# Kernel optimization log

Hardware: AMD Instinct MI355X
Metric: run time of the kernel (lower is better)

Reference implementation:

```python
import jax, jax.numpy as jnp
import numpy as np

B, S, H, NH = 2, 2048, 2048, 16
HD = H // NH
SCALE = 1.0 / np.sqrt(HD).astype(np.float32)


def setup_inputs() -> dict:
    key = jax.random.key(0)
    ks = jax.random.split(key, 11)
    std = 1.0 / np.sqrt(H)
    inp = {
        'query': jax.random.normal(ks[0], (B, S, H), dtype=jnp.float32),
        'key': jax.random.normal(ks[1], (B, S, H), dtype=jnp.float32),
        'value': jax.random.normal(ks[2], (B, S, H), dtype=jnp.float32),
        'Wq': jax.random.normal(ks[3], (H, H), dtype=jnp.float32) * std,
        'bq': jax.random.normal(ks[4], (H,), dtype=jnp.float32) * std,
        'Wk': jax.random.normal(ks[5], (H, H), dtype=jnp.float32) * std,
        'bk': jax.random.normal(ks[6], (H,), dtype=jnp.float32) * std,
        'Wv': jax.random.normal(ks[7], (H, H), dtype=jnp.float32) * std,
        'bv': jax.random.normal(ks[8], (H,), dtype=jnp.float32) * std,
        'Wo': jax.random.normal(ks[9], (H, H), dtype=jnp.float32) * std,
        'bo': jax.random.normal(ks[10], (H,), dtype=jnp.float32) * std,
    }
    return inp


def reference(query, key, value, Wq, bq, Wk, bk, Wv, bv, Wo, bo):
    # Linear projections (torch Linear: x @ W.T + b)
    q = query @ Wq.T + bq
    k = key @ Wk.T + bk
    v = value @ Wv.T + bv
    # [B, NH, S, HD]
    q = q.reshape(B, S, NH, HD).transpose(0, 2, 1, 3)
    k = k.reshape(B, S, NH, HD).transpose(0, 2, 1, 3)
    v = v.reshape(B, S, NH, HD).transpose(0, 2, 1, 3)
    scores = jnp.einsum('bhqd,bhkd->bhqk', q, k) * SCALE
    attn = jax.nn.softmax(scores, axis=-1)  # dropout p=0 (eval)
    ctx = jnp.einsum('bhqk,bhkd->bhqd', attn, v)
    ctx = ctx.transpose(0, 2, 1, 3).reshape(B, S, H)
    out = ctx @ Wo.T + bo
    return out
```

## Files before the change

kernel.cpp:

```cpp
#include <hip/hip_runtime.h>


typedef __bf16 bf16_t;
typedef __bf16 bf16x8 __attribute__((ext_vector_type(8)));
typedef float  f32x4  __attribute__((ext_vector_type(4)));

#define DEVI __device__ __forceinline__

DEVI void async_copy16(const void* gsrc, void* ldst) {
  __builtin_amdgcn_global_load_lds(
      (const __attribute__((address_space(1))) unsigned int*)gsrc,
      (__attribute__((address_space(3))) unsigned int*)ldst, 16, 0, 0);
}

constexpr int Bc = 2, Sc = 2048, Hc = 2048, NHc = 16, HDc = 128;
constexpr float SCALE_F = 0.088388347648318447f;
constexpr int PSTR = 136;

DEVI void cast_body(const float* __restrict__ in, bf16_t* __restrict__ out) {
  int i = (blockIdx.x * 256 + threadIdx.x) * 8;
  float4 f0 = *(const float4*)(in + i);
  float4 f1 = *(const float4*)(in + i + 4);
  union { bf16_t h[8]; uint4 u; } o;
  o.h[0] = (bf16_t)f0.x; o.h[1] = (bf16_t)f0.y;
  o.h[2] = (bf16_t)f0.z; o.h[3] = (bf16_t)f0.w;
  o.h[4] = (bf16_t)f1.x; o.h[5] = (bf16_t)f1.y;
  o.h[6] = (bf16_t)f1.z; o.h[7] = (bf16_t)f1.w;
  *(uint4*)(out + i) = o.u;
}

__global__ void cast3(const float* __restrict__ a, const float* __restrict__ b,
                      const float* __restrict__ c, bf16_t* __restrict__ oa,
                      bf16_t* __restrict__ ob, bf16_t* __restrict__ oc) {
  const float* src = blockIdx.y == 0 ? a : blockIdx.y == 1 ? b : c;
  bf16_t* dst = blockIdx.y == 0 ? oa : blockIdx.y == 1 ? ob : oc;
  cast_body(src, dst);
}

__global__ void cast4(const float* __restrict__ a, const float* __restrict__ b,
                      const float* __restrict__ c, const float* __restrict__ d,
                      bf16_t* __restrict__ oa, bf16_t* __restrict__ ob,
                      bf16_t* __restrict__ oc, bf16_t* __restrict__ od) {
  const float* src = blockIdx.y == 0 ? a : blockIdx.y == 1 ? b
                   : blockIdx.y == 2 ? c : d;
  bf16_t* dst = blockIdx.y == 0 ? oa : blockIdx.y == 1 ? ob
              : blockIdx.y == 2 ? oc : od;
  cast_body(src, dst);
}

template <int M, int N, int K, int OUT_MODE>
__global__ __launch_bounds__(256, 2) void gemm_bt(const bf16_t* __restrict__ A,
                                                  const bf16_t* __restrict__ Bw,
                                                  const float* __restrict__ bias,
                                                  void* __restrict__ Cout,
                                                  float scale) {
  constexpr int BM = 128, BN = 128, BK = 64;
  __shared__ __align__(16) bf16_t As[BM * BK];
  __shared__ __align__(16) bf16_t Bs[BN * BK];
  const int tid = threadIdx.x;
  const int lane = tid & 63;
  const int wave = tid >> 6;
  const int bm = blockIdx.x & (M / BM - 1);
  const int bn = blockIdx.x / (M / BM);
  const int wm = wave >> 1, wn = wave & 1;
  const int quad = lane >> 4, l15 = lane & 15;

  int s_r[4], s_c[4];
#pragma unroll
  for (int i = 0; i < 4; ++i) {
    int seg = wave * 4 + i;
    int r = seg * 8 + (lane >> 3);
    s_r[i] = r;
    s_c[i] = (lane & 7) ^ (r & 7);
  }
  const bf16_t* Abase = A + (size_t)bm * BM * K;
  const bf16_t* Bbase = Bw + (size_t)bn * BN * K;

  f32x4 zero4 = {0.f, 0.f, 0.f, 0.f};
  f32x4 acc[4][4];
#pragma unroll
  for (int i = 0; i < 4; ++i)
#pragma unroll
    for (int j = 0; j < 4; ++j) acc[i][j] = zero4;

  int arow[4], brow[4];
#pragma unroll
  for (int t = 0; t < 4; ++t) {
    arow[t] = wm * 64 + t * 16 + l15;
    brow[t] = wn * 64 + t * 16 + l15;
  }

  for (int kt = 0; kt < K / BK; ++kt) {
    const int k0 = kt * BK;
#pragma unroll
    for (int i = 0; i < 4; ++i) {
      int seg = wave * 4 + i;
      async_copy16(Abase + (size_t)s_r[i] * K + k0 + s_c[i] * 8, As + seg * 512);
      async_copy16(Bbase + (size_t)s_r[i] * K + k0 + s_c[i] * 8, Bs + seg * 512);
    }
    __syncthreads();
#pragma unroll
    for (int ks = 0; ks < 2; ++ks) {
      bf16x8 af[4], bfv[4];
#pragma unroll
      for (int mt = 0; mt < 4; ++mt)
        af[mt] = *(const bf16x8*)(As + arow[mt] * 64 +
                                  (((ks * 4 + quad) ^ (arow[mt] & 7)) * 8));
#pragma unroll
      for (int nt = 0; nt < 4; ++nt)
        bfv[nt] = *(const bf16x8*)(Bs + brow[nt] * 64 +
                                   (((ks * 4 + quad) ^ (brow[nt] & 7)) * 8));
#pragma unroll
      for (int mt = 0; mt < 4; ++mt)
#pragma unroll
        for (int nt = 0; nt < 4; ++nt)
          acc[mt][nt] = __builtin_amdgcn_mfma_f32_16x16x32_bf16(
              af[mt], bfv[nt], acc[mt][nt], 0, 0, 0);
    }
    __syncthreads();
  }

  float bv[4];
#pragma unroll
  for (int nt = 0; nt < 4; ++nt) bv[nt] = bias[bn * BN + brow[nt]];

#pragma unroll
  for (int mt = 0; mt < 4; ++mt) {
    const int rbase = bm * BM + wm * 64 + mt * 16 + quad * 4;
#pragma unroll
    for (int nt = 0; nt < 4; ++nt) {
      const int col = bn * BN + brow[nt];
      if constexpr (OUT_MODE == 0) {
        bf16_t* C = (bf16_t*)Cout;
#pragma unroll
        for (int r = 0; r < 4; ++r)
          C[(size_t)(rbase + r) * N + col] = (bf16_t)((acc[mt][nt][r] + bv[nt]) * scale);
      } else if constexpr (OUT_MODE == 2) {
        float* C = (float*)Cout;
#pragma unroll
        for (int r = 0; r < 4; ++r)
          C[(size_t)(rbase + r) * N + col] = acc[mt][nt][r] + bv[nt];
      } else {
        bf16_t* C = (bf16_t*)Cout;
        const int bb = rbase >> 11;
        const int s0 = rbase & (Sc - 1);
        const int h = col >> 7, d = col & (HDc - 1);
        union { bf16_t h4[4]; uint2 u; } o;
#pragma unroll
        for (int r = 0; r < 4; ++r) o.h4[r] = (bf16_t)(acc[mt][nt][r] + bv[nt]);
        *(uint2*)(C + (((size_t)(bb * NHc + h) * HDc + d) * Sc + s0)) = o.u;
      }
    }
  }
}

__global__ __launch_bounds__(256, 1) void flash_attn(const bf16_t* __restrict__ Q,
                                                     const bf16_t* __restrict__ Kg,
                                                     const bf16_t* __restrict__ Vt,
                                                     bf16_t* __restrict__ ctx) {
  extern __shared__ char smem[];
  bf16_t* Ks = (bf16_t*)smem;
  bf16_t* Vs = (bf16_t*)(smem + 32768);
  bf16_t* Ps = (bf16_t*)(smem + 65536);

  const int tid = threadIdx.x, lane = tid & 63, wave = tid >> 6;
  const int quad = lane >> 4, l15 = lane & 15;
  const int bid = blockIdx.x;
  const int qt = bid & 15, h = (bid >> 4) & 15, b = bid >> 8;

  bf16_t* Pw = Ps + wave * (32 * PSTR);

  bf16x8 qf[2][4];
#pragma unroll
  for (int mt = 0; mt < 2; ++mt) {
    int grow = b * Sc + qt * 128 + wave * 32 + mt * 16 + l15;
    const bf16_t* qp = Q + (size_t)grow * Hc + h * HDc;
#pragma unroll
    for (int kc = 0; kc < 4; ++kc) qf[mt][kc] = *(const bf16x8*)(qp + kc * 32 + quad * 8);
  }

  f32x4 zero4 = {0.f, 0.f, 0.f, 0.f};
  f32x4 o[2][8];
#pragma unroll
  for (int mt = 0; mt < 2; ++mt)
#pragma unroll
    for (int dt = 0; dt < 8; ++dt) o[mt][dt] = zero4;
  float mrow[2][4], lrow[2][4];
#pragma unroll
  for (int mt = 0; mt < 2; ++mt)
#pragma unroll
    for (int r = 0; r < 4; ++r) { mrow[mt][r] = -1e30f; lrow[mt][r] = 0.f; }

  int st_r[8], st_c[8];
#pragma unroll
  for (int i = 0; i < 8; ++i) {
    int seg = wave * 8 + i;
    st_r[i] = seg * 4 + (lane >> 4);
    st_c[i] = (lane & 15) ^ (st_r[i] & 7);
  }
  const bf16_t* Kbase = Kg + (size_t)b * Sc * Hc + h * HDc;
  const bf16_t* Vbase = Vt + (size_t)(b * NHc + h) * HDc * Sc;

  for (int kb = 0; kb < 16; ++kb) {
#pragma unroll
    for (int i = 0; i < 8; ++i) {
      int seg = wave * 8 + i;
      async_copy16(Kbase + (size_t)(kb * 128 + st_r[i]) * Hc + st_c[i] * 8, Ks + seg * 512);
      async_copy16(Vbase + (size_t)st_r[i] * Sc + kb * 128 + st_c[i] * 8, Vs + seg * 512);
    }
    __syncthreads();

    f32x4 sf[2][8];
#pragma unroll
    for (int mt = 0; mt < 2; ++mt)
#pragma unroll
      for (int nt = 0; nt < 8; ++nt) sf[mt][nt] = zero4;
#pragma unroll
    for (int kc = 0; kc < 4; ++kc)
#pragma unroll
      for (int nt = 0; nt < 8; ++nt) {
        int kr = nt * 16 + l15;
        bf16x8 kf = *(const bf16x8*)(Ks + kr * 128 + (((kc * 4 + quad) ^ (kr & 7)) * 8));
        sf[0][nt] = __builtin_amdgcn_mfma_f32_16x16x32_bf16(qf[0][kc], kf, sf[0][nt], 0, 0, 0);
        sf[1][nt] = __builtin_amdgcn_mfma_f32_16x16x32_bf16(qf[1][kc], kf, sf[1][nt], 0, 0, 0);
      }

#pragma unroll
    for (int mt = 0; mt < 2; ++mt)
#pragma unroll
      for (int r = 0; r < 4; ++r) {
        float mx = sf[mt][0][r];
#pragma unroll
        for (int nt = 1; nt < 8; ++nt) mx = fmaxf(mx, sf[mt][nt][r]);
#pragma unroll
        for (int off = 1; off < 16; off <<= 1) mx = fmaxf(mx, __shfl_xor(mx, off));
        float mnew = fmaxf(mrow[mt][r], mx);
        float alpha = __expf(mrow[mt][r] - mnew);
        float rs = 0.f;
#pragma unroll
        for (int nt = 0; nt < 8; ++nt) {
          float p = __expf(sf[mt][nt][r] - mnew);
          sf[mt][nt][r] = p;
          rs += p;
        }
#pragma unroll
        for (int off = 1; off < 16; off <<= 1) rs += __shfl_xor(rs, off);
        lrow[mt][r] = lrow[mt][r] * alpha + rs;
        mrow[mt][r] = mnew;
#pragma unroll
        for (int dt = 0; dt < 8; ++dt) o[mt][dt][r] *= alpha;
      }

#pragma unroll
    for (int mt = 0; mt < 2; ++mt)
#pragma unroll
      for (int nt = 0; nt < 8; ++nt)
#pragma unroll
        for (int r = 0; r < 4; ++r)
          Pw[(mt * 16 + quad * 4 + r) * PSTR + nt * 16 + l15] = (bf16_t)sf[mt][nt][r];

    bf16x8 pf[2][4];
#pragma unroll
    for (int mt = 0; mt < 2; ++mt) {
      const bf16_t* pr = Pw + (mt * 16 + l15) * PSTR;
#pragma unroll
      for (int kc = 0; kc < 4; ++kc)
        pf[mt][kc] = *(const bf16x8*)(pr + kc * 32 + quad * 8);
    }

#pragma unroll
    for (int kc = 0; kc < 4; ++kc)
#pragma unroll
      for (int dt = 0; dt < 8; ++dt) {
        int vr = dt * 16 + l15;
        bf16x8 vf = *(const bf16x8*)(Vs + vr * 128 + (((kc * 4 + quad) ^ (vr & 7)) * 8));
        o[0][dt] = __builtin_amdgcn_mfma_f32_16x16x32_bf16(pf[0][kc], vf, o[0][dt], 0, 0, 0);
        o[1][dt] = __builtin_amdgcn_mfma_f32_16x16x32_bf16(pf[1][kc], vf, o[1][dt], 0, 0, 0);
      }
    __syncthreads();
  }

#pragma unroll
  for (int mt = 0; mt < 2; ++mt) {
    float rinv[4];
#pragma unroll
    for (int r = 0; r < 4; ++r) rinv[r] = 1.f / lrow[mt][r];
#pragma unroll
    for (int dt = 0; dt < 8; ++dt)
#pragma unroll
      for (int r = 0; r < 4; ++r)
        Pw[(mt * 16 + quad * 4 + r) * PSTR + dt * 16 + l15] = (bf16_t)(o[mt][dt][r] * rinv[r]);
  }
#pragma unroll
  for (int r = 0; r < 32; ++r) {
    unsigned v = *(const unsigned*)(Pw + r * PSTR + lane * 2);
    int grow = b * Sc + qt * 128 + wave * 32 + r;
    *(unsigned*)(ctx + (size_t)grow * Hc + h * HDc + lane * 2) = v;
  }
}

extern "C" void kernel_launch(void* const* d_in, const int* in_sizes, int n_in,
                              void* d_out, int out_size, void* d_ws, size_t ws_size,
                              hipStream_t stream) {
  const float* query = (const float*)d_in[0];
  const float* key_i = (const float*)d_in[1];
  const float* value = (const float*)d_in[2];
  const float* Wq = (const float*)d_in[3];
  const float* bq = (const float*)d_in[4];
  const float* Wk = (const float*)d_in[5];
  const float* bk = (const float*)d_in[6];
  const float* Wv = (const float*)d_in[7];
  const float* bv = (const float*)d_in[8];
  const float* Wo = (const float*)d_in[9];
  const float* bo = (const float*)d_in[10];

  const size_t XE = (size_t)Bc * Sc * Hc;
  const size_t WE = (size_t)Hc * Hc;
  const size_t need = 6 * XE * 2 + 4 * WE * 2;
  if (ws_size < need) return;

  char* ws = (char*)d_ws;
  size_t off = 0;
  auto alloc = [&](size_t bytes) {
    char* p = ws + off;
    off += (bytes + 255) & ~(size_t)255;
    return p;
  };
  bf16_t* Xq = (bf16_t*)alloc(XE * 2);
  bf16_t* Xk = (bf16_t*)alloc(XE * 2);
  bf16_t* Xv = (bf16_t*)alloc(XE * 2);
  bf16_t* Wqb = (bf16_t*)alloc(WE * 2);
  bf16_t* Wkb = (bf16_t*)alloc(WE * 2);
  bf16_t* Wvb = (bf16_t*)alloc(WE * 2);
  bf16_t* Wob = (bf16_t*)alloc(WE * 2);
  bf16_t* qb = (bf16_t*)alloc(XE * 2);
  bf16_t* kb = (bf16_t*)alloc(XE * 2);
  bf16_t* vtb = (bf16_t*)alloc(XE * 2);
  bf16_t* ctxb = Xq;

  cast3<<<dim3((unsigned)(XE / 2048), 3), 256, 0, stream>>>(query, key_i, value, Xq, Xk, Xv);
  cast4<<<dim3((unsigned)(WE / 2048), 4), 256, 0, stream>>>(Wq, Wk, Wv, Wo, Wqb, Wkb, Wvb, Wob);

  gemm_bt<4096, 2048, 2048, 0><<<512, 256, 0, stream>>>(Xq, Wqb, bq, qb, SCALE_F);
  gemm_bt<4096, 2048, 2048, 0><<<512, 256, 0, stream>>>(Xk, Wkb, bk, kb, 1.0f);
  gemm_bt<4096, 2048, 2048, 1><<<512, 256, 0, stream>>>(Xv, Wvb, bv, vtb, 1.0f);

  hipFuncSetAttribute((const void*)flash_attn,
                      hipFuncAttributeMaxDynamicSharedMemorySize, 100352);
  flash_attn<<<512, 256, 100352, stream>>>(qb, kb, vtb, ctxb);

  gemm_bt<4096, 2048, 2048, 2><<<512, 256, 0, stream>>>(ctxb, Wob, bo, (float*)d_out, 1.0f);
}
```

Measured before the change: 502.3 us.

## Halve flash-attention KV tile to 64 to fit two blocks per CU

Shrinks the K/V tile per iteration from 128 to 64 keys, which cuts shared memory from about 98KB to about 50KB (static allocation) and raises launch bounds to two blocks per CU. The epilogue now reuses the K/V region for output staging after an extra barrier. The goal is higher occupancy so that one block's loads and barriers overlap with another block's MFMA work. In exchange the loop runs twice as many iterations, each with its own barriers and softmax rescaling, and the tighter register budget may cause spills.

```diff
diff --git a/kernel.cpp b/kernel.cpp
--- a/kernel.cpp
+++ b/kernel.cpp
@@ -15,7 +15,7 @@
 
 constexpr int Bc = 2, Sc = 2048, Hc = 2048, NHc = 16, HDc = 128;
 constexpr float SCALE_F = 0.088388347648318447f;
-constexpr int PSTR = 136;
+constexpr int PSTR = 72;
 
 DEVI void cast_body(const float* __restrict__ in, bf16_t* __restrict__ out) {
   int i = (blockIdx.x * 256 + threadIdx.x) * 8;
@@ -154,14 +154,14 @@
   }
 }
 
-__global__ __launch_bounds__(256, 1) void flash_attn(const bf16_t* __restrict__ Q,
+__global__ __launch_bounds__(256, 2) void flash_attn(const bf16_t* __restrict__ Q,
                                                      const bf16_t* __restrict__ Kg,
                                                      const bf16_t* __restrict__ Vt,
                                                      bf16_t* __restrict__ ctx) {
-  extern __shared__ char smem[];
-  bf16_t* Ks = (bf16_t*)smem;
-  bf16_t* Vs = (bf16_t*)(smem + 32768);
-  bf16_t* Ps = (bf16_t*)(smem + 65536);
+  __shared__ __align__(16) bf16_t smem[64 * 128 + 128 * 64 + 4 * 32 * PSTR];
+  bf16_t* Ks = smem;
+  bf16_t* Vs = smem + 8192;
+  bf16_t* Ps = smem + 16384;
 
   const int tid = threadIdx.x, lane = tid & 63, wave = tid >> 6;
   const int quad = lane >> 4, l15 = lane & 15;
@@ -191,34 +191,34 @@
 #pragma unroll
     for (int r = 0; r < 4; ++r) { mrow[mt][r] = -1e30f; lrow[mt][r] = 0.f; }
 
-  int st_r[8], st_c[8];
-#pragma unroll
-  for (int i = 0; i < 8; ++i) {
-    int seg = wave * 8 + i;
-    st_r[i] = seg * 4 + (lane >> 4);
-    st_c[i] = (lane & 15) ^ (st_r[i] & 7);
+  int kr_[4], kc_[4], vr_[4], vc_[4];
+#pragma unroll
+  for (int i = 0; i < 4; ++i) {
+    int s = wave * 4 + i;
+    kr_[i] = s * 4 + quad;        kc_[i] = l15 ^ (kr_[i] & 7);
+    vr_[i] = s * 8 + (lane >> 3); vc_[i] = (lane & 7) ^ (vr_[i] & 7);
   }
   const bf16_t* Kbase = Kg + (size_t)b * Sc * Hc + h * HDc;
   const bf16_t* Vbase = Vt + (size_t)(b * NHc + h) * HDc * Sc;
 
-  for (int kb = 0; kb < 16; ++kb) {
-#pragma unroll
-    for (int i = 0; i < 8; ++i) {
-      int seg = wave * 8 + i;
-      async_copy16(Kbase + (size_t)(kb * 128 + st_r[i]) * Hc + st_c[i] * 8, Ks + seg * 512);
-      async_copy16(Vbase + (size_t)st_r[i] * Sc + kb * 128 + st_c[i] * 8, Vs + seg * 512);
+  for (int kb = 0; kb < 32; ++kb) {
+#pragma unroll
+    for (int i = 0; i < 4; ++i) {
+      int s = wave * 4 + i;
+      async_copy16(Kbase + (size_t)(kb * 64 + kr_[i]) * Hc + kc_[i] * 8, Ks + s * 512);
+      async_copy16(Vbase + (size_t)vr_[i] * Sc + kb * 64 + vc_[i] * 8, Vs + s * 512);
     }
     __syncthreads();
 
-    f32x4 sf[2][8];
+    f32x4 sf[2][4];
 #pragma unroll
     for (int mt = 0; mt < 2; ++mt)
 #pragma unroll
-      for (int nt = 0; nt < 8; ++nt) sf[mt][nt] = zero4;
+      for (int nt = 0; nt < 4; ++nt) sf[mt][nt] = zero4;
 #pragma unroll
     for (int kc = 0; kc < 4; ++kc)
 #pragma unroll
-      for (int nt = 0; nt < 8; ++nt) {
+      for (int nt = 0; nt < 4; ++nt) {
         int kr = nt * 16 + l15;
         bf16x8 kf = *(const bf16x8*)(Ks + kr * 128 + (((kc * 4 + quad) ^ (kr & 7)) * 8));
         sf[0][nt] = __builtin_amdgcn_mfma_f32_16x16x32_bf16(qf[0][kc], kf, sf[0][nt], 0, 0, 0);
@@ -231,14 +231,14 @@
       for (int r = 0; r < 4; ++r) {
         float mx = sf[mt][0][r];
 #pragma unroll
-        for (int nt = 1; nt < 8; ++nt) mx = fmaxf(mx, sf[mt][nt][r]);
+        for (int nt = 1; nt < 4; ++nt) mx = fmaxf(mx, sf[mt][nt][r]);
 #pragma unroll
         for (int off = 1; off < 16; off <<= 1) mx = fmaxf(mx, __shfl_xor(mx, off));
         float mnew = fmaxf(mrow[mt][r], mx);
         float alpha = __expf(mrow[mt][r] - mnew);
         float rs = 0.f;
 #pragma unroll
-        for (int nt = 0; nt < 8; ++nt) {
+        for (int nt = 0; nt < 4; ++nt) {
           float p = __expf(sf[mt][nt][r] - mnew);
           sf[mt][nt][r] = p;
           rs += p;
@@ -254,32 +254,34 @@
 #pragma unroll
     for (int mt = 0; mt < 2; ++mt)
 #pragma unroll
-      for (int nt = 0; nt < 8; ++nt)
+      for (int nt = 0; nt < 4; ++nt)
 #pragma unroll
         for (int r = 0; r < 4; ++r)
           Pw[(mt * 16 + quad * 4 + r) * PSTR + nt * 16 + l15] = (bf16_t)sf[mt][nt][r];
 
-    bf16x8 pf[2][4];
+    bf16x8 pf[2][2];
 #pragma unroll
     for (int mt = 0; mt < 2; ++mt) {
       const bf16_t* pr = Pw + (mt * 16 + l15) * PSTR;
 #pragma unroll
-      for (int kc = 0; kc < 4; ++kc)
+      for (int kc = 0; kc < 2; ++kc)
         pf[mt][kc] = *(const bf16x8*)(pr + kc * 32 + quad * 8);
     }
 
 #pragma unroll
-    for (int kc = 0; kc < 4; ++kc)
+    for (int kc = 0; kc < 2; ++kc)
 #pragma unroll
       for (int dt = 0; dt < 8; ++dt) {
         int vr = dt * 16 + l15;
-        bf16x8 vf = *(const bf16x8*)(Vs + vr * 128 + (((kc * 4 + quad) ^ (vr & 7)) * 8));
+        bf16x8 vf = *(const bf16x8*)(Vs + vr * 64 + (((kc * 4 + quad) ^ (vr & 7)) * 8));
         o[0][dt] = __builtin_amdgcn_mfma_f32_16x16x32_bf16(pf[0][kc], vf, o[0][dt], 0, 0, 0);
         o[1][dt] = __builtin_amdgcn_mfma_f32_16x16x32_bf16(pf[1][kc], vf, o[1][dt], 0, 0, 0);
       }
     __syncthreads();
   }
 
+  __syncthreads();
+  bf16_t* Ow = smem + wave * 4096;
 #pragma unroll
   for (int mt = 0; mt < 2; ++mt) {
     float rinv[4];
@@ -289,11 +291,11 @@
     for (int dt = 0; dt < 8; ++dt)
 #pragma unroll
       for (int r = 0; r < 4; ++r)
-        Pw[(mt * 16 + quad * 4 + r) * PSTR + dt * 16 + l15] = (bf16_t)(o[mt][dt][r] * rinv[r]);
+        Ow[(mt * 16 + quad * 4 + r) * 128 + dt * 16 + l15] = (bf16_t)(o[mt][dt][r] * rinv[r]);
   }
 #pragma unroll
   for (int r = 0; r < 32; ++r) {
-    unsigned v = *(const unsigned*)(Pw + r * PSTR + lane * 2);
+    unsigned v = *(const unsigned*)(Ow + r * 128 + lane * 2);
     int grow = b * Sc + qt * 128 + wave * 32 + r;
     *(unsigned*)(ctx + (size_t)grow * Hc + h * HDc + lane * 2) = v;
   }
@@ -345,9 +347,7 @@
   gemm_bt<4096, 2048, 2048, 0><<<512, 256, 0, stream>>>(Xk, Wkb, bk, kb, 1.0f);
   gemm_bt<4096, 2048, 2048, 1><<<512, 256, 0, stream>>>(Xv, Wvb, bv, vtb, 1.0f);
 
-  hipFuncSetAttribute((const void*)flash_attn,
-                      hipFuncAttributeMaxDynamicSharedMemorySize, 100352);
-  flash_attn<<<512, 256, 100352, stream>>>(qb, kb, vtb, ctxb);
+  flash_attn<<<512, 256, 0, stream>>>(qb, kb, vtb, ctxb);
 
   gemm_bt<4096, 2048, 2048, 2><<<512, 256, 0, stream>>>(ctxb, Wob, bo, (float*)d_out, 1.0f);
 }
```

New measurement: 477.8 us. 4.9% less time.
